# Kernel tuning notes

Hardware: AMD Instinct MI355X
Metric: run time of the kernel (lower is better)

Reference implementation:

```python
import jax, jax.numpy as jnp
import numpy as np

B, S, H, O = 256, 2048, 64, 2


def setup_inputs() -> dict:
    key = jax.random.key(0)
    ks = jax.random.split(key, 13)
    s = 1.0 / np.sqrt(H)
    return {
        "x": jax.random.normal(ks[0], (B, S, 2), jnp.float32),
        "h_0": jax.random.normal(ks[1], (1, B, H), jnp.float32),
        "Wa": jax.random.normal(ks[2], (1 + H, H), jnp.float32) * s,
        "ba": jax.random.normal(ks[3], (H,), jnp.float32) * s,
        "Wp1": jax.random.normal(ks[4], (1 + H, H), jnp.float32) * s,
        "bp1": jax.random.normal(ks[5], (H,), jnp.float32) * s,
        "Wp2": jax.random.normal(ks[6], (1 + H, H), jnp.float32) * s,
        "bp2": jax.random.normal(ks[7], (H,), jnp.float32) * s,
        "Wz": jax.random.normal(ks[8], (2 * H, H), jnp.float32) * s,
        "bz": jax.random.normal(ks[9], (H,), jnp.float32) * s,
        "Wh": jax.random.normal(ks[10], (2 * H, H), jnp.float32) * s,
        "bh": jax.random.normal(ks[11], (H,), jnp.float32) * s,
        "W_out": jax.random.normal(ks[12], (H, O), jnp.float32) * s,
        "b_out": jnp.zeros((O,), jnp.float32),
    }


def reference(x, h_0, Wa, ba, Wp1, bp1, Wp2, bp2, Wz, bz, Wh, bh, W_out, b_out):
    # I/Q -> amplitude & phase (precompute outside scan)
    i_x, q_x = x[..., 0], x[..., 1]           # [B,S]
    amp = jnp.sqrt(i_x * i_x + q_x * q_x)     # [B,S]
    ang = jnp.arctan2(q_x, i_x)               # [B,S]
    cos_a = jnp.cos(ang)
    sin_a = jnp.sin(ang)

    # Split weights: first row acts on the scalar input, rest on h.
    def step(h, inp):
        a_t, c_t, s_t = inp                   # each [B]
        a_n = jnp.tanh(a_t[:, None] * Wa[0] + h @ Wa[1:] + ba)
        p1 = jnp.tanh(c_t[:, None] * Wp1[0] + h @ Wp1[1:] + bp1)
        p2 = jnp.tanh(s_t[:, None] * Wp2[0] + h @ Wp2[1:] + bp2)
        u = a_n * p1 * p2 * (1 - a_n) * (1 - p1) * (1 - p2)
        z = jax.nn.sigmoid(u @ Wz[:H] + h @ Wz[H:] + bz)
        h_cand = jnp.tanh(u @ Wh[:H] + h @ Wh[H:] + bh)
        h_new = z * h + (1 - z) * h_cand
        return h_new, h_new

    xs = (amp.T, cos_a.T, sin_a.T)            # time-major [S,B]
    _, hs = jax.lax.scan(step, h_0[0], xs)    # hs: [S,B,H]
    out = jnp.transpose(hs, (1, 0, 2))        # [B,S,H]
    return out @ W_out + b_out                # [B,S,O]
```

## Files before the change

### kernel.cpp

```cpp
#include <hip/hip_runtime.h>

#define SS 2048
#define HH 64

typedef _Float16 h2v __attribute__((ext_vector_type(2)));
typedef unsigned int uint;

__device__ __forceinline__ float fdot2f(uint w, uint x, float c) {
#if __has_builtin(__builtin_amdgcn_fdot2)
    return __builtin_amdgcn_fdot2(__builtin_bit_cast(h2v, w),
                                  __builtin_bit_cast(h2v, x), c, false);
#else
    h2v a = __builtin_bit_cast(h2v, w), bb = __builtin_bit_cast(h2v, x);
    return fmaf((float)a[0], (float)bb[0], fmaf((float)a[1], (float)bb[1], c));
#endif
}
__device__ __forceinline__ uint pack2(float a, float b) {
    h2v v = {(_Float16)a, (_Float16)b};
    return __builtin_bit_cast(uint, v);
}
__device__ __forceinline__ unsigned short f16bits(float a) {
    return __builtin_bit_cast(unsigned short, (_Float16)a);
}
__device__ __forceinline__ float fast_tanh(float x) {
    float ax = fabsf(x);
    float e = __expf(-2.0f * ax);
    float r = (1.0f - e) * __builtin_amdgcn_rcpf(1.0f + e);
    return copysignf(r, x);
}
__device__ __forceinline__ float fast_sigmoid(float x) {
    return __builtin_amdgcn_rcpf(1.0f + __expf(-x));
}

__global__ __launch_bounds__(128)
__attribute__((amdgpu_waves_per_eu(1, 1)))
void pgjanet_kernel(
    const float* __restrict__ x,
    const float* __restrict__ h0,
    const float* __restrict__ Wa,
    const float* __restrict__ ba,
    const float* __restrict__ Wp1,
    const float* __restrict__ bp1,
    const float* __restrict__ Wp2,
    const float* __restrict__ bp2,
    const float* __restrict__ Wz,
    const float* __restrict__ bz,
    const float* __restrict__ Wh,
    const float* __restrict__ bh,
    const float* __restrict__ Wout,
    const float* __restrict__ bout,
    float* __restrict__ out)
{
    const int b   = blockIdx.x;
    const int tid = threadIdx.x;
    const int j   = tid & 63;
    const int w   = tid >> 6;

    __shared__ float2 xs2[SS];
    __shared__ __align__(16) unsigned short hpkW[2][64];
    __shared__ __align__(16) unsigned short upk[64];
    __shared__ __align__(8) float2 zhhhL[2][64];
    __shared__ __align__(8) float2 szshL[2][2][64];
    __shared__ float hbufL[32 * 65];
    __shared__ float WoutT[2 * 68];

    {
        const float2* xb = (const float2*)(x + (size_t)b * SS * 2);
        #pragma unroll
        for (int it = 0; it < SS / 128; ++it)
            xs2[tid + it * 128] = xb[tid + it * 128];
    }
    float bo_ = 0.f;
    if (w == 1) {
        WoutT[0 * 68 + j] = Wout[j * 2 + 0];
        WoutT[1 * 68 + j] = Wout[j * 2 + 1];
        bo_ = bout[j & 1];
    }

    float w0a = 0.f, baR = 0.f, w0p1 = 0.f, bp1R = 0.f, w0p2 = 0.f, bp2R = 0.f;
    if (w == 0) {
        w0a = Wa[j];  baR  = ba[j];
        w0p1 = Wp1[j]; bp1R = bp1[j];
        w0p2 = Wp2[j]; bp2R = bp2[j];
    }
    const float bzR = bz[j], bhR = bh[j];

    const float* src0;
    const float* src1;
    const float* src2;
    if (w == 0) { src0 = Wa + HH;      src1 = Wp1 + HH;     src2 = Wp2 + HH; }
    else        { src0 = Wz + 64 * HH; src1 = Wh + 64 * HH; src2 = Wz + 64 * HH; }

    uint wph1[96];
    #pragma unroll
    for (int p = 0; p < 32; ++p) {
        wph1[p]      = pack2(src0[(2 * p) * HH + j], src0[(2 * p + 1) * HH + j]);
        wph1[32 + p] = pack2(src1[(2 * p) * HH + j], src1[(2 * p + 1) * HH + j]);
        wph1[64 + p] = pack2(src2[(2 * p) * HH + j], src2[(2 * p + 1) * HH + j]);
    }
    uint wZ2[16], wH2[16];
    {
        const int kb = 32 * w;
        #pragma unroll
        for (int p = 0; p < 16; ++p) {
            wZ2[p] = pack2(Wz[(kb + 2 * p) * HH + j], Wz[(kb + 2 * p + 1) * HH + j]);
            wH2[p] = pack2(Wh[(kb + 2 * p) * HH + j], Wh[(kb + 2 * p + 1) * HH + j]);
        }
    }
    #pragma unroll
    for (int k = 0; k < 96; ++k) asm volatile("" : "+v"(wph1[k]));
    #pragma unroll
    for (int k = 0; k < 16; ++k) asm volatile("" : "+a"(wZ2[k]), "+a"(wH2[k]));

    float hreg = h0[b * HH + j];
    hpkW[w][j] = f16bits(hreg);

    float amp = 0.f, ca = 0.f, sa = 0.f;
    if (w == 0) {
        const float2 xt = xs2[0];
        const float d = xt.x * xt.x + xt.y * xt.y;
        const float inv = (d > 0.f) ? __builtin_amdgcn_rsqf(d) : 0.f;
        amp = d * inv;
        ca  = (d > 0.f) ? xt.x * inv : 1.0f;
        sa  = xt.y * inv;
    }

    __syncthreads();

    for (int t = 0; t < SS; ++t) {
        const int par = t & 1;

        uint hp[32];
        {
            const uint4* hp4 = (const uint4*)hpkW[w];
            #pragma unroll
            for (int g = 0; g < 8; ++g) {
                uint4 v = hp4[g];
                hp[4*g+0] = v.x; hp[4*g+1] = v.y;
                hp[4*g+2] = v.z; hp[4*g+3] = v.w;
            }
        }

        float zh_r = 0.f, hh_r = 0.f;
        if (w == 0) {
            float aA0 = 0.f, aA1 = 0.f, aP10 = 0.f, aP11 = 0.f, aP20 = 0.f, aP21 = 0.f;
            #pragma unroll
            for (int g = 0; g < 8; ++g) {
                aA0  = fdot2f(wph1[4*g+0],      hp[4*g+0], aA0);
                aA1  = fdot2f(wph1[4*g+1],      hp[4*g+1], aA1);
                aA0  = fdot2f(wph1[4*g+2],      hp[4*g+2], aA0);
                aA1  = fdot2f(wph1[4*g+3],      hp[4*g+3], aA1);
                aP10 = fdot2f(wph1[32+4*g+0],   hp[4*g+0], aP10);
                aP11 = fdot2f(wph1[32+4*g+1],   hp[4*g+1], aP11);
                aP10 = fdot2f(wph1[32+4*g+2],   hp[4*g+2], aP10);
                aP11 = fdot2f(wph1[32+4*g+3],   hp[4*g+3], aP11);
                aP20 = fdot2f(wph1[64+4*g+0],   hp[4*g+0], aP20);
                aP21 = fdot2f(wph1[64+4*g+1],   hp[4*g+1], aP21);
                aP20 = fdot2f(wph1[64+4*g+2],   hp[4*g+2], aP20);
                aP21 = fdot2f(wph1[64+4*g+3],   hp[4*g+3], aP21);
            }
            const float a_  = fast_tanh(aA0 + aA1 + fmaf(amp, w0a,  baR));
            const float p1_ = fast_tanh(aP10 + aP11 + fmaf(ca, w0p1, bp1R));
            const float p2_ = fast_tanh(aP20 + aP21 + fmaf(sa, w0p2, bp2R));
            const float u = a_ * p1_ * p2_ * (1.f - a_) * (1.f - p1_) * (1.f - p2_);
            upk[j] = f16bits(u);
        } else {
            float z0 = 0.f, z1 = 0.f, h0r = 0.f, h1r = 0.f;
            #pragma unroll
            for (int g = 0; g < 8; ++g) {
                z0  = fdot2f(wph1[4*g+0],    hp[4*g+0], z0);
                z1  = fdot2f(wph1[4*g+1],    hp[4*g+1], z1);
                z0  = fdot2f(wph1[4*g+2],    hp[4*g+2], z0);
                z1  = fdot2f(wph1[4*g+3],    hp[4*g+3], z1);
                h0r = fdot2f(wph1[32+4*g+0], hp[4*g+0], h0r);
                h1r = fdot2f(wph1[32+4*g+1], hp[4*g+1], h1r);
                h0r = fdot2f(wph1[32+4*g+2], hp[4*g+2], h0r);
                h1r = fdot2f(wph1[32+4*g+3], hp[4*g+3], h1r);
            }
            zh_r = z0 + z1;
            hh_r = h0r + h1r;
            zhhhL[par][j] = make_float2(zh_r, hh_r);
        }
        __syncthreads();

        float2 zhhh_w0 = make_float2(0.f, 0.f);
        if (w == 0) zhhh_w0 = zhhhL[par][j];

        float sz, sh;
        {
            uint up[16];
            {
                const uint4* up4 = (const uint4*)(upk + 32 * w);
                #pragma unroll
                for (int g = 0; g < 4; ++g) {
                    uint4 v = up4[g];
                    up[4*g+0] = v.x; up[4*g+1] = v.y;
                    up[4*g+2] = v.z; up[4*g+3] = v.w;
                }
            }
            if (w == 0) {
                const float2 xn = xs2[(t + 1) & (SS - 1)];
                const float dn = xn.x * xn.x + xn.y * xn.y;
                const float invn = (dn > 0.f) ? __builtin_amdgcn_rsqf(dn) : 0.f;
                amp = dn * invn;
                ca  = (dn > 0.f) ? xn.x * invn : 1.0f;
                sa  = xn.y * invn;
            }
            float sz0 = 0.f, sz1 = 0.f, sh0 = 0.f, sh1 = 0.f;
            #pragma unroll
            for (int p = 0; p < 16; p += 2) {
                sz0 = fdot2f(wZ2[p + 0], up[p + 0], sz0);
                sz1 = fdot2f(wZ2[p + 1], up[p + 1], sz1);
                sh0 = fdot2f(wH2[p + 0], up[p + 0], sh0);
                sh1 = fdot2f(wH2[p + 1], up[p + 1], sh1);
            }
            sz = sz0 + sz1;
            sh = sh0 + sh1;
            szshL[w][par][j] = make_float2(sz, sh);
        }
        __syncthreads();

        {
            float zh_t, hh_t;
            float2 o;
            if (w == 0) {
                zh_t = zhhh_w0.x; hh_t = zhhh_w0.y;
                o = szshL[1][par][j];
            } else {
                zh_t = zh_r; hh_t = hh_r;
                o = szshL[0][par][j];
            }
            const float z  = fast_sigmoid(sz + o.x + zh_t + bzR);
            const float hc = fast_tanh(sh + o.y + hh_t + bhR);
            hreg = fmaf(z, hreg - hc, hc);
            hpkW[w][j] = f16bits(hreg);
        }

        if (w == 1) {
            hbufL[(t & 31) * 65 + j] = hreg;
            if ((t & 31) == 31) {
                const int r = j >> 1, o2 = j & 1;
                float acc = 0.f;
                #pragma unroll
                for (int k = 0; k < 64; ++k)
                    acc += hbufL[r * 65 + k] * WoutT[o2 * 68 + k];
                out[((size_t)b * SS + (t - 31 + r)) * 2 + o2] = acc + bo_;
            }
        }
    }
}

extern "C" void kernel_launch(void* const* d_in, const int* in_sizes, int n_in,
                              void* d_out, int out_size, void* d_ws, size_t ws_size,
                              hipStream_t stream) {
    const float* x    = (const float*)d_in[0];
    const float* h0   = (const float*)d_in[1];
    const float* Wa   = (const float*)d_in[2];
    const float* ba   = (const float*)d_in[3];
    const float* Wp1  = (const float*)d_in[4];
    const float* bp1  = (const float*)d_in[5];
    const float* Wp2  = (const float*)d_in[6];
    const float* bp2  = (const float*)d_in[7];
    const float* Wz   = (const float*)d_in[8];
    const float* bz   = (const float*)d_in[9];
    const float* Wh   = (const float*)d_in[10];
    const float* bh   = (const float*)d_in[11];
    const float* Wout = (const float*)d_in[12];
    const float* bout = (const float*)d_in[13];
    float* out = (float*)d_out;

    pgjanet_kernel<<<256, 128, 0, stream>>>(x, h0, Wa, ba, Wp1, bp1, Wp2, bp2,
                                            Wz, bz, Wh, bh, Wout, bout, out);
}
```

Before: 1.439 ms.

## Rebalance u-projection between waves and defer output projection off critical path

Wave 0 now handles 40 of the 64 u-columns of the Wz/Wh projection, taking u values straight from registers via readlane rather than a shared-memory round trip, while wave 1 handles the remaining 24 from LDS. The 32-step output projection block moves into wave 1's first phase, where it overlaps with wave 0's heavier gate work, and a final flush handles the last block. This aims to balance per-step work between the two waves and shorten the serial step latency, at the cost of many readlane instructions and extra accumulation registers.

```diff
diff --git a/kernel.cpp b/kernel.cpp
--- a/kernel.cpp
+++ b/kernel.cpp
@@ -6,6 +6,9 @@
 typedef _Float16 h2v __attribute__((ext_vector_type(2)));
 typedef unsigned int uint;
 
+__device__ __forceinline__ float readlane_f(float v, int l) {
+    return __int_as_float(__builtin_amdgcn_readlane(__float_as_int(v), l));
+}
 __device__ __forceinline__ float fdot2f(uint w, uint x, float c) {
 #if __has_builtin(__builtin_amdgcn_fdot2)
     return __builtin_amdgcn_fdot2(__builtin_bit_cast(h2v, w),
@@ -98,19 +101,26 @@
         wph1[32 + p] = pack2(src1[(2 * p) * HH + j], src1[(2 * p + 1) * HH + j]);
         wph1[64 + p] = pack2(src2[(2 * p) * HH + j], src2[(2 * p + 1) * HH + j]);
     }
-    uint wZ2[16], wH2[16];
-    {
-        const int kb = 32 * w;
-        #pragma unroll
-        for (int p = 0; p < 16; ++p) {
-            wZ2[p] = pack2(Wz[(kb + 2 * p) * HH + j], Wz[(kb + 2 * p + 1) * HH + j]);
-            wH2[p] = pack2(Wh[(kb + 2 * p) * HH + j], Wh[(kb + 2 * p + 1) * HH + j]);
-        }
+    uint wZ2[20], wH2[20];
+    if (w == 0) {
+        #pragma unroll
+        for (int p = 0; p < 20; ++p) {
+            wZ2[p] = pack2(Wz[(2 * p) * HH + j], Wz[(2 * p + 1) * HH + j]);
+            wH2[p] = pack2(Wh[(2 * p) * HH + j], Wh[(2 * p + 1) * HH + j]);
+        }
+    } else {
+        #pragma unroll
+        for (int p = 0; p < 12; ++p) {
+            wZ2[p] = pack2(Wz[(40 + 2 * p) * HH + j], Wz[(41 + 2 * p) * HH + j]);
+            wH2[p] = pack2(Wh[(40 + 2 * p) * HH + j], Wh[(41 + 2 * p) * HH + j]);
+        }
+        #pragma unroll
+        for (int p = 12; p < 20; ++p) { wZ2[p] = 0u; wH2[p] = 0u; }
     }
     #pragma unroll
     for (int k = 0; k < 96; ++k) asm volatile("" : "+v"(wph1[k]));
     #pragma unroll
-    for (int k = 0; k < 16; ++k) asm volatile("" : "+a"(wZ2[k]), "+a"(wH2[k]));
+    for (int k = 0; k < 20; ++k) asm volatile("" : "+a"(wZ2[k]), "+a"(wH2[k]));
 
     float hreg = h0[b * HH + j];
     hpkW[w][j] = f16bits(hreg);
@@ -141,6 +151,7 @@
             }
         }
 
+        float u_w0 = 0.f;
         float zh_r = 0.f, hh_r = 0.f;
         if (w == 0) {
             float aA0 = 0.f, aA1 = 0.f, aP10 = 0.f, aP11 = 0.f, aP20 = 0.f, aP21 = 0.f;
@@ -162,8 +173,8 @@
             const float a_  = fast_tanh(aA0 + aA1 + fmaf(amp, w0a,  baR));
             const float p1_ = fast_tanh(aP10 + aP11 + fmaf(ca, w0p1, bp1R));
             const float p2_ = fast_tanh(aP20 + aP21 + fmaf(sa, w0p2, bp2R));
-            const float u = a_ * p1_ * p2_ * (1.f - a_) * (1.f - p1_) * (1.f - p2_);
-            upk[j] = f16bits(u);
+            u_w0 = a_ * p1_ * p2_ * (1.f - a_) * (1.f - p1_) * (1.f - p2_);
+            upk[j] = f16bits(u_w0);
         } else {
             float z0 = 0.f, z1 = 0.f, h0r = 0.f, h1r = 0.f;
             #pragma unroll
@@ -180,6 +191,15 @@
             zh_r = z0 + z1;
             hh_r = h0r + h1r;
             zhhhL[par][j] = make_float2(zh_r, hh_r);
+
+            if ((t & 31) == 0 && t > 0) {
+                const int r = j >> 1, o2 = j & 1;
+                float acc = 0.f;
+                #pragma unroll
+                for (int k = 0; k < 64; ++k)
+                    acc += hbufL[r * 65 + k] * WoutT[o2 * 68 + k];
+                out[((size_t)b * SS + (t - 32 + r)) * 2 + o2] = acc + bo_;
+            }
         }
         __syncthreads();
 
@@ -187,18 +207,18 @@
         if (w == 0) zhhh_w0 = zhhhL[par][j];
 
         float sz, sh;
-        {
-            uint up[16];
+        if (w == 0) {
+            float sz0 = 0.f, sz1 = 0.f, sh0 = 0.f, sh1 = 0.f;
+            #pragma unroll
+            for (int p = 0; p < 20; p += 2) {
+                const uint ua = pack2(readlane_f(u_w0, 2*p),     readlane_f(u_w0, 2*p + 1));
+                const uint ub = pack2(readlane_f(u_w0, 2*p + 2), readlane_f(u_w0, 2*p + 3));
+                sz0 = fdot2f(wZ2[p + 0], ua, sz0);
+                sz1 = fdot2f(wZ2[p + 1], ub, sz1);
+                sh0 = fdot2f(wH2[p + 0], ua, sh0);
+                sh1 = fdot2f(wH2[p + 1], ub, sh1);
+            }
             {
-                const uint4* up4 = (const uint4*)(upk + 32 * w);
-                #pragma unroll
-                for (int g = 0; g < 4; ++g) {
-                    uint4 v = up4[g];
-                    up[4*g+0] = v.x; up[4*g+1] = v.y;
-                    up[4*g+2] = v.z; up[4*g+3] = v.w;
-                }
-            }
-            if (w == 0) {
                 const float2 xn = xs2[(t + 1) & (SS - 1)];
                 const float dn = xn.x * xn.x + xn.y * xn.y;
                 const float invn = (dn > 0.f) ? __builtin_amdgcn_rsqf(dn) : 0.f;
@@ -206,9 +226,22 @@
                 ca  = (dn > 0.f) ? xn.x * invn : 1.0f;
                 sa  = xn.y * invn;
             }
+            sz = sz0 + sz1;
+            sh = sh0 + sh1;
+        } else {
+            uint up[12];
+            {
+                const uint4* up4 = (const uint4*)(upk + 40);
+                #pragma unroll
+                for (int g = 0; g < 3; ++g) {
+                    uint4 v = up4[g];
+                    up[4*g+0] = v.x; up[4*g+1] = v.y;
+                    up[4*g+2] = v.z; up[4*g+3] = v.w;
+                }
+            }
             float sz0 = 0.f, sz1 = 0.f, sh0 = 0.f, sh1 = 0.f;
             #pragma unroll
-            for (int p = 0; p < 16; p += 2) {
+            for (int p = 0; p < 12; p += 2) {
                 sz0 = fdot2f(wZ2[p + 0], up[p + 0], sz0);
                 sz1 = fdot2f(wZ2[p + 1], up[p + 1], sz1);
                 sh0 = fdot2f(wH2[p + 0], up[p + 0], sh0);
@@ -216,8 +249,8 @@
             }
             sz = sz0 + sz1;
             sh = sh0 + sh1;
-            szshL[w][par][j] = make_float2(sz, sh);
-        }
+        }
+        szshL[w][par][j] = make_float2(sz, sh);
         __syncthreads();
 
         {
@@ -236,17 +269,16 @@
             hpkW[w][j] = f16bits(hreg);
         }
 
-        if (w == 1) {
-            hbufL[(t & 31) * 65 + j] = hreg;
-            if ((t & 31) == 31) {
-                const int r = j >> 1, o2 = j & 1;
-                float acc = 0.f;
-                #pragma unroll
-                for (int k = 0; k < 64; ++k)
-                    acc += hbufL[r * 65 + k] * WoutT[o2 * 68 + k];
-                out[((size_t)b * SS + (t - 31 + r)) * 2 + o2] = acc + bo_;
-            }
-        }
+        if (w == 1) hbufL[(t & 31) * 65 + j] = hreg;
+    }
+
+    if (w == 1) {
+        const int r = j >> 1, o2 = j & 1;
+        float acc = 0.f;
+        #pragma unroll
+        for (int k = 0; k < 64; ++k)
+            acc += hbufL[r * 65 + k] * WoutT[o2 * 68 + k];
+        out[((size_t)b * SS + (SS - 32 + r)) * 2 + o2] = acc + bo_;
     }
 }
 
```

Result: slower. 1.783 ms (+23.9%).
